# Kernel optimization log

Measured on AMD Instinct MI355X. Metric: run time of the kernel, lower is better.

The kernel has to match this reference:

```python
import jax, jax.numpy as jnp
import numpy as np

B, T_DEC, T_ENC = 64, 2048, 512
G_STEPS = 20000          # guided_att_steps
GAMMA = 0.99995          # guided_att_gamma


def setup_inputs() -> dict:
    key = jax.random.key(0)
    k1, k2, k3 = jax.random.split(key, 3)
    alignments = jax.random.uniform(k1, (B, T_DEC, T_ENC), dtype=jnp.float32)
    # ragged lengths in [dim/2, dim] (avoid zero-length -> div by zero)
    input_lengths = jax.random.randint(k2, (B,), T_ENC // 2, T_ENC + 1, dtype=jnp.int32)
    target_lengths = jax.random.randint(k3, (B,), T_DEC // 2, T_DEC + 1, dtype=jnp.int32)
    return {
        "alignments": alignments,
        "input_lengths": input_lengths,
        "target_lengths": target_lengths,
        "global_step": 10000,
    }


def reference(alignments, input_lengths, target_lengths, global_step):
    # matches torch: if self._g_steps < global_step: return 0
    if G_STEPS < global_step:
        return jnp.zeros((), dtype=alignments.dtype)
    g = GAMMA ** global_step  # python float constant
    inv_denom = 1.0 / (2.0 * g * g)

    F = target_lengths.astype(jnp.float32)[:, None, None]   # [B,1,1]
    L = input_lengths.astype(jnp.float32)[:, None, None]    # [B,1,1]
    f = jnp.arange(T_DEC, dtype=jnp.float32)[None, :, None]  # [1,T_dec,1]
    l = jnp.arange(T_ENC, dtype=jnp.float32)[None, None, :]  # [1,1,T_enc]

    # ragged diagonal gaussian mask, zero outside valid [f<F, l<L] region
    w = 1.0 - jnp.exp(-((l / L - f / F) ** 2) * inv_denom)   # [B,T_dec,T_enc]
    valid = (f < F) & (l < L)
    w = jnp.where(valid, w, 0.0)

    per_sample = jnp.sum(w * alignments, axis=(1, 2))        # [B]
    loss = jnp.mean(per_sample / target_lengths.astype(jnp.float32))
    return loss
```

## Files before the change

### kernel.cpp

```cpp
#include <hip/hip_runtime.h>


#define BB     64
#define TDEC   2048
#define TENC   512
#define GSTEPS 20000
#define GAMMA  0.99995
#define SLABS  32
#define SLAB_ROWS (TDEC / SLABS)
#define LOG2E  1.4426950408889634f

__global__ void gal_prologue(const int* __restrict__ step_p,
                             float* __restrict__ ws,
                             float* __restrict__ out) {
    int step = step_p[0];
    double g = 1.0, base = GAMMA;
    unsigned e = (step > 0) ? (unsigned)step : 0u;
    while (e) {
        if (e & 1u) g *= base;
        base *= base;
        e >>= 1;
    }
    ws[0] = (float)(1.0 / (2.0 * g * g));
    ((int*)ws)[1] = (GSTEPS < step) ? 0 : 1;
    out[0] = 0.0f;
}

__global__ __launch_bounds__(256) void gal_main(
    const float* __restrict__ align,
    const int* __restrict__ in_len,
    const int* __restrict__ tgt_len,
    const float* __restrict__ ws,
    float* __restrict__ out) {

    const int b          = blockIdx.x >> 5;
    const int slab       = blockIdx.x & (SLABS - 1);
    const int slab_start = slab * SLAB_ROWS;

    const float inv_denom = ws[0];
    const int   active    = ((const int*)ws)[1];

    const int F = tgt_len[b];
    const int L = in_len[b];

    float acc = 0.0f;

    const int rows_end = min(slab_start + SLAB_ROWS, F);
    const int nrows    = rows_end - slab_start;

    if (active && nrows > 0) {
        const int tid = threadIdx.x;
        const int col = tid & 127;
        const int r   = tid >> 7;
        const int l0  = col << 2;

        const float invF = 1.0f / (float)F;
        const float invL = 1.0f / (float)L;
        const float c    = -inv_denom * LOG2E;

        float lv[4], cm[4];
        #pragma unroll
        for (int j = 0; j < 4; ++j) {
            const int l = l0 + j;
            lv[j] = (float)l * invL;
            cm[j] = (l < L) ? 1.0f : 0.0f;
        }

        const float4* p = (const float4*)(align + ((size_t)b * TDEC + slab_start + r) * TENC) + col;
        const int nev = nrows & ~1;

        #pragma unroll 4
        for (int k = 0; k < nev; k += 2) {
            const float4 a  = *p;
            const float  fd = (float)(slab_start + k + r) * invF;
            #pragma unroll
            for (int j = 0; j < 4; ++j) {
                const float d   = lv[j] - fd;
                const float e   = __builtin_amdgcn_exp2f((d * c) * d);
                const float am  = (&a.x)[j] * cm[j];
                acc += am;
                acc  = fmaf(-e, am, acc);
            }
            p += 2 * (TENC / 4);
        }

        if ((nrows & 1) && r == 0) {
            const float4 a  = *p;
            const float  fd = (float)(rows_end - 1) * invF;
            #pragma unroll
            for (int j = 0; j < 4; ++j) {
                const float d  = lv[j] - fd;
                const float e  = __builtin_amdgcn_exp2f((d * c) * d);
                const float am = (&a.x)[j] * cm[j];
                acc += am;
                acc  = fmaf(-e, am, acc);
            }
        }

        acc *= invF * (1.0f / (float)BB);
    }

    #pragma unroll
    for (int off = 32; off > 0; off >>= 1) acc += __shfl_down(acc, off, 64);
    __shared__ float swave[4];
    const int lane = threadIdx.x & 63;
    const int wid  = threadIdx.x >> 6;
    if (lane == 0) swave[wid] = acc;
    __syncthreads();
    if (threadIdx.x == 0) {
        atomicAdd(out, swave[0] + swave[1] + swave[2] + swave[3]);
    }
}

extern "C" void kernel_launch(void* const* d_in, const int* in_sizes, int n_in,
                              void* d_out, int out_size, void* d_ws, size_t ws_size,
                              hipStream_t stream) {
    const float* align   = (const float*)d_in[0];
    const int*   in_len  = (const int*)d_in[1];
    const int*   tgt_len = (const int*)d_in[2];
    const int*   step_p  = (const int*)d_in[3];
    float* out = (float*)d_out;
    float* ws  = (float*)d_ws;

    gal_prologue<<<1, 1, 0, stream>>>(step_p, ws, out);

    gal_main<<<BB * SLABS, 256, 0, stream>>>(align, in_len, tgt_len, ws, out);
}
```

Before: 347.6 us.

## Skip out-of-range columns, fold prologue into main, reduce partials deterministically

Threads whose four encoder columns all lie beyond the sample's input length now skip loading alignments entirely. The gamma power is computed inside the main kernel, so the separate single-thread prologue launch goes away. The global atomicAdd is replaced by per-block partial sums written to workspace and summed by a small epilogue kernel. The aim is to cut memory traffic for padded columns and avoid atomic contention, at the cost of redundant per-block double-precision pow work.

```diff
diff --git a/kernel.cpp b/kernel.cpp
--- a/kernel.cpp
+++ b/kernel.cpp
@@ -8,12 +8,10 @@
 #define GAMMA  0.99995
 #define SLABS  32
 #define SLAB_ROWS (TDEC / SLABS)
+#define NBLK   (BB * SLABS)
 #define LOG2E  1.4426950408889634f
 
-__global__ void gal_prologue(const int* __restrict__ step_p,
-                             float* __restrict__ ws,
-                             float* __restrict__ out) {
-    int step = step_p[0];
+__device__ inline double gal_pow_gamma(int step) {
     double g = 1.0, base = GAMMA;
     unsigned e = (step > 0) ? (unsigned)step : 0u;
     while (e) {
@@ -21,24 +19,22 @@
         base *= base;
         e >>= 1;
     }
-    ws[0] = (float)(1.0 / (2.0 * g * g));
-    ((int*)ws)[1] = (GSTEPS < step) ? 0 : 1;
-    out[0] = 0.0f;
+    return g;
 }
 
 __global__ __launch_bounds__(256) void gal_main(
     const float* __restrict__ align,
     const int* __restrict__ in_len,
     const int* __restrict__ tgt_len,
-    const float* __restrict__ ws,
-    float* __restrict__ out) {
+    const int* __restrict__ step_p,
+    float* __restrict__ partials) {
 
     const int b          = blockIdx.x >> 5;
     const int slab       = blockIdx.x & (SLABS - 1);
     const int slab_start = slab * SLAB_ROWS;
 
-    const float inv_denom = ws[0];
-    const int   active    = ((const int*)ws)[1];
+    const int step   = step_p[0];
+    const int active = (GSTEPS < step) ? 0 : 1;
 
     const int F = tgt_len[b];
     const int L = in_len[b];
@@ -48,11 +44,14 @@
     const int rows_end = min(slab_start + SLAB_ROWS, F);
     const int nrows    = rows_end - slab_start;
 
-    if (active && nrows > 0) {
-        const int tid = threadIdx.x;
-        const int col = tid & 127;
-        const int r   = tid >> 7;
-        const int l0  = col << 2;
+    const int tid = threadIdx.x;
+    const int col = tid & 127;
+    const int r   = tid >> 7;
+    const int l0  = col << 2;
+
+    if (active && nrows > 0 && l0 < L) {
+        const double g = gal_pow_gamma(step);
+        const float inv_denom = (float)(1.0 / (2.0 * g * g));
 
         const float invF = 1.0f / (float)F;
         const float invL = 1.0f / (float)L;
@@ -75,9 +74,9 @@
             const float  fd = (float)(slab_start + k + r) * invF;
             #pragma unroll
             for (int j = 0; j < 4; ++j) {
-                const float d   = lv[j] - fd;
-                const float e   = __builtin_amdgcn_exp2f((d * c) * d);
-                const float am  = (&a.x)[j] * cm[j];
+                const float d  = lv[j] - fd;
+                const float e  = __builtin_amdgcn_exp2f((d * c) * d);
+                const float am = (&a.x)[j] * cm[j];
                 acc += am;
                 acc  = fmaf(-e, am, acc);
             }
@@ -108,7 +107,33 @@
     if (lane == 0) swave[wid] = acc;
     __syncthreads();
     if (threadIdx.x == 0) {
-        atomicAdd(out, swave[0] + swave[1] + swave[2] + swave[3]);
+        partials[blockIdx.x] = swave[0] + swave[1] + swave[2] + swave[3];
+    }
+}
+
+__global__ __launch_bounds__(256) void gal_epilogue(
+    const float* __restrict__ partials,
+    const int* __restrict__ step_p,
+    float* __restrict__ out) {
+
+    const int step   = step_p[0];
+    const int active = (GSTEPS < step) ? 0 : 1;
+
+    float acc = 0.0f;
+    if (active) {
+        #pragma unroll
+        for (int k = 0; k < NBLK / 256; ++k)
+            acc += partials[k * 256 + threadIdx.x];
+    }
+    #pragma unroll
+    for (int off = 32; off > 0; off >>= 1) acc += __shfl_down(acc, off, 64);
+    __shared__ float swave[4];
+    const int lane = threadIdx.x & 63;
+    const int wid  = threadIdx.x >> 6;
+    if (lane == 0) swave[wid] = acc;
+    __syncthreads();
+    if (threadIdx.x == 0) {
+        out[0] = swave[0] + swave[1] + swave[2] + swave[3];
     }
 }
 
@@ -119,10 +144,9 @@
     const int*   in_len  = (const int*)d_in[1];
     const int*   tgt_len = (const int*)d_in[2];
     const int*   step_p  = (const int*)d_in[3];
-    float* out = (float*)d_out;
-    float* ws  = (float*)d_ws;
+    float* out      = (float*)d_out;
+    float* partials = (float*)d_ws;
 
-    gal_prologue<<<1, 1, 0, stream>>>(step_p, ws, out);
-
-    gal_main<<<BB * SLABS, 256, 0, stream>>>(align, in_len, tgt_len, ws, out);
+    gal_main<<<NBLK, 256, 0, stream>>>(align, in_len, tgt_len, step_p, partials);
+    gal_epilogue<<<1, 256, 0, stream>>>(partials, step_p, out);
 }
```

After: 334.2 us. -3.9%, faster.
